# Optimization experiments

Measured on AMD Instinct MI355X. Metric: run time of the kernel, lower is better.

## Reference

```python
import jax, jax.numpy as jnp
import numpy as np

B, L, H, W = 16, 4096, 64, 64
SEQ = 1024  # target_sequence_length (hardcoded in the torch module)
SP = 32     # sqrt(SEQ)


def _conv1d(x, w, b, pad):
    y = jax.lax.conv_general_dilated(x, w, (1,), [(pad, pad)],
                                     dimension_numbers=('NCH', 'OIH', 'NCH'))
    return y + b[None, :, None]


def _conv2d(x, w, b, pad, groups=1):
    y = jax.lax.conv_general_dilated(x, w, (1, 1), [(pad, pad)] * 2,
                                     feature_group_count=groups,
                                     dimension_numbers=('NCHW', 'OIHW', 'NCHW'))
    return y + b[None, :, None, None]


def _forward(us_input, img_input, us_w1, us_b1, us_w2, us_b2, us_w3, us_b3,
             aff_w, aff_w_high, aff_thr, img_w1, img_b1, img_w2, img_b2, img_w3, img_b3,
             db_qkv_w, db_qkv_b, db_dw_w, db_dw_b, db_proj_w, db_proj_b,
             db_fc_w, db_fc_b, db_dep_w, db_dep_b, db_temp,
             ca_qkv_w, ca_qkv_b, ca_out_w, ca_out_b,
             tf_ch1_w, tf_ch1_b, tf_ch2_w, tf_ch2_b,
             tf_sp1_w, tf_sp1_b, tf_sp2_w, tf_sp2_b, cls_w, cls_b):
    b = us_input.shape[0]
    # ---- ultrasound 1D conv branch ----
    x = us_input.transpose(0, 2, 1)                    # [B,1,L]
    x = jax.nn.relu(_conv1d(x, us_w1, us_b1, 1))
    x = jax.nn.relu(_conv1d(x, us_w2, us_b2, 1))
    x = jax.nn.relu(_conv1d(x, us_w3, us_b3, 1))
    us_feat = x.transpose(0, 2, 1)                     # [B,L,64]
    # ---- adaptive frequency filtering (training-mode high-freq mask included) ----
    n = us_feat.shape[1]
    xf = jnp.fft.rfft(us_feat, axis=1, norm='ortho')   # [B,Nf,64] complex
    w_c = aff_w[:, 0] + 1j * aff_w[:, 1]
    xw = xf * w_c
    energy = jnp.sum(jnp.abs(xf) ** 2, axis=-1)        # [B,Nf]
    med = jnp.median(energy.reshape(b, -1), axis=1, keepdims=True)
    ne = energy / (med + 1e-6)
    hard = (ne > aff_thr).astype(jnp.float32)
    mask = jax.lax.stop_gradient(hard - aff_thr) + aff_thr  # straight-through threshold
    wh_c = aff_w_high[:, 0] + 1j * aff_w_high[:, 1]
    xw = xw + (xf * mask[..., None]) * wh_c
    us_feat = jnp.fft.irfft(xw, n=n, axis=1, norm='ortho')  # [B,L,64]
    # ---- image 2D conv branch ----
    y = jax.nn.relu(_conv2d(img_input, img_w1, img_b1, 1))
    y = jax.nn.relu(_conv2d(y, img_w2, img_b2, 1))
    y = jax.nn.relu(_conv2d(y, img_w3, img_b3, 1))     # [B,64,H,W]
    # ---- dual-branch feature fusion block ----
    hgt, wid = y.shape[2], y.shape[3]
    hw = hgt * wid
    qkv = jnp.einsum('oi,bihw->bohw', db_qkv_w, y) + db_qkv_b[None, :, None, None]
    qkv = _conv2d(qkv, db_dw_w, db_dw_b, 1, groups=192)      # depthwise (3x3x3 conv @ D=1 -> center 3x3)
    # convolutional branch: faithful row-major reshape as in torch
    f_all = qkv.reshape(b, hw, 12, 16).transpose(0, 2, 1, 3)  # [B,12,HW,16]
    f_all = jnp.einsum('oi,bink->bonk', db_fc_w, f_all) + db_fc_b[None, :, None, None]
    f_conv = f_all.transpose(0, 3, 1, 2).reshape(b, 144, hgt, wid)
    out_conv = _conv2d(f_conv, db_dep_w, db_dep_b, 1, groups=16)  # [B,64,H,W]
    # channel attention branch
    q, k, v = jnp.split(qkv, 3, axis=1)
    q = q.reshape(b, 4, 16, hw)
    k = k.reshape(b, 4, 16, hw)
    v = v.reshape(b, 4, 16, hw)
    q = q / jnp.maximum(jnp.linalg.norm(q, axis=-1, keepdims=True), 1e-12)
    k = k / jnp.maximum(jnp.linalg.norm(k, axis=-1, keepdims=True), 1e-12)
    attn = jax.nn.softmax(jnp.einsum('bhcn,bhdn->bhcd', q, k) * db_temp, axis=-1)
    out = jnp.einsum('bhcd,bhdn->bhcn', attn, v).reshape(b, 64, hgt, wid)
    out = jnp.einsum('oi,bihw->bohw', db_proj_w, out) + db_proj_b[None, :, None, None]
    img_feat = (out + out_conv).reshape(b, 64, hw).transpose(0, 2, 1)  # [B,HW,64]
    # ---- adaptive avg pool to SEQ (lengths divide evenly) ----
    us_red = us_feat.transpose(0, 2, 1).reshape(b, 64, SEQ, -1).mean(-1).transpose(0, 2, 1)
    img_red = img_feat.transpose(0, 2, 1).reshape(b, 64, SEQ, -1).mean(-1).transpose(0, 2, 1)
    # ---- cross-modal attention (shared qkv/out projections) ----
    def heads(t):
        u = (jnp.einsum('bli,oi->blo', t, ca_qkv_w) + ca_qkv_b).reshape(b, SEQ, 4, 3, 16)
        return (u[:, :, :, 0].transpose(0, 2, 1, 3),
                u[:, :, :, 1].transpose(0, 2, 1, 3),
                u[:, :, :, 2].transpose(0, 2, 1, 3))
    q1, k1, v1 = heads(us_red)
    q2, k2, v2 = heads(img_red)
    scale = 1.0 / jnp.sqrt(jnp.float32(16.0))
    a1 = jax.nn.softmax(jnp.einsum('bhqd,bhkd->bhqk', q1, k2) * scale, axis=-1)
    a2 = jax.nn.softmax(jnp.einsum('bhqd,bhkd->bhqk', q2, k1) * scale, axis=-1)
    o1 = jnp.einsum('bhqk,bhkd->bhqd', a1, v2).transpose(0, 2, 1, 3).reshape(b, SEQ, 64)
    o2 = jnp.einsum('bhqk,bhkd->bhqd', a2, v1).transpose(0, 2, 1, 3).reshape(b, SEQ, 64)
    o1 = jnp.einsum('bli,oi->blo', o1, ca_out_w) + ca_out_b
    o2 = jnp.einsum('bli,oi->blo', o2, ca_out_w) + ca_out_b
    t1 = o1.transpose(0, 2, 1).reshape(b, 64, SP, SP)
    t2 = o2.transpose(0, 2, 1).reshape(b, 64, SP, SP)
    # ---- modal fusion attention (channel + spatial gating) ----
    ch_pool = jnp.stack([t1.mean((2, 3)), t1.max((2, 3)), t2.mean((2, 3)), t2.max((2, 3))], axis=1)  # [B,4,64]
    c1 = _conv1d(ch_pool, tf_ch1_w, tf_ch1_b, 1)      # [B,1,64]
    c2 = _conv1d(ch_pool, tf_ch2_w, tf_ch2_b, 1)
    ch_stack = jax.nn.softmax(jnp.stack([c1, c2], 0), axis=0)      # [2,B,1,64]
    ch_stack = ch_stack.transpose(0, 1, 3, 2)[..., None]           # [2,B,64,1,1]
    sp_pool = jnp.concatenate([t1.mean(1, keepdims=True), t1.max(1, keepdims=True),
                               t2.mean(1, keepdims=True), t2.max(1, keepdims=True)], axis=1)
    s1 = _conv2d(sp_pool, tf_sp1_w, tf_sp1_b, 3)
    s2 = _conv2d(sp_pool, tf_sp2_w, tf_sp2_b, 3)
    sp_stack = jax.nn.softmax(jnp.stack([s1, s2], 0), axis=0)      # [2,B,1,SP,SP]
    att = ch_stack + sp_stack + 1.0                                # [2,B,64,SP,SP]
    fuse = att[0] * t1 + att[1] * t2
    logits = fuse.mean((2, 3)) @ cls_w.T + cls_b
    return jax.nn.softmax(logits, axis=1)


def setup_inputs() -> dict:
    key = jax.random.key(0)
    ks = iter(jax.random.split(key, 64))
    def rn(shape, s=0.2):
        return jax.random.normal(next(ks), shape, dtype=jnp.float32) * s
    d = {
        'us_input': jax.random.normal(next(ks), (B, L, 1), dtype=jnp.float32),
        'img_input': jax.random.normal(next(ks), (B, 3, H, W), dtype=jnp.float32),
        'us_w1': rn((16, 1, 3)), 'us_b1': rn((16,), 0.02),
        'us_w2': rn((32, 16, 3)), 'us_b2': rn((32,), 0.02),
        'us_w3': rn((64, 32, 3)), 'us_b3': rn((64,), 0.02),
        'aff_w': rn((64, 2), 0.02), 'aff_w_high': rn((64, 2), 0.02),
        'aff_thr': jax.random.uniform(next(ks), (1,), dtype=jnp.float32),
        'img_w1': rn((16, 3, 3, 3)), 'img_b1': rn((16,), 0.02),
        'img_w2': rn((32, 16, 3, 3)), 'img_b2': rn((32,), 0.02),
        'img_w3': rn((64, 32, 3, 3)), 'img_b3': rn((64,), 0.02),
        'db_qkv_w': rn((192, 64), 0.1), 'db_qkv_b': rn((192,), 0.02),
        'db_dw_w': rn((192, 1, 3, 3)), 'db_dw_b': rn((192,), 0.02),
        'db_proj_w': rn((64, 64), 0.1), 'db_proj_b': rn((64,), 0.02),
        'db_fc_w': rn((9, 12), 0.1), 'db_fc_b': rn((9,), 0.02),
        'db_dep_w': rn((64, 9, 3, 3), 0.1), 'db_dep_b': rn((64,), 0.02),
        'db_temp': jnp.ones((4, 1, 1), dtype=jnp.float32),
        'ca_qkv_w': rn((192, 64), 0.1), 'ca_qkv_b': rn((192,), 0.02),
        'ca_out_w': rn((64, 64), 0.1), 'ca_out_b': rn((64,), 0.02),
        'tf_ch1_w': rn((1, 4, 3)), 'tf_ch1_b': rn((1,), 0.02),
        'tf_ch2_w': rn((1, 4, 3)), 'tf_ch2_b': rn((1,), 0.02),
        'tf_sp1_w': rn((1, 4, 7, 7)), 'tf_sp1_b': rn((1,), 0.02),
        'tf_sp2_w': rn((1, 4, 7, 7)), 'tf_sp2_b': rn((1,), 0.02),
        'cls_w': rn((9, 64), 0.1), 'cls_b': rn((9,), 0.02),
    }
    return d


def reference(us_input, img_input, us_w1, us_b1, us_w2, us_b2, us_w3, us_b3,
              aff_w, aff_w_high, aff_thr, img_w1, img_b1, img_w2, img_b2, img_w3, img_b3,
              db_qkv_w, db_qkv_b, db_dw_w, db_dw_b, db_proj_w, db_proj_b,
              db_fc_w, db_fc_b, db_dep_w, db_dep_b, db_temp,
              ca_qkv_w, ca_qkv_b, ca_out_w, ca_out_b,
              tf_ch1_w, tf_ch1_b, tf_ch2_w, tf_ch2_b,
              tf_sp1_w, tf_sp1_b, tf_sp2_w, tf_sp2_b, cls_w, cls_b):
    return _forward(us_input, img_input, us_w1, us_b1, us_w2, us_b2, us_w3, us_b3,
                    aff_w, aff_w_high, aff_thr, img_w1, img_b1, img_w2, img_b2, img_w3, img_b3,
                    db_qkv_w, db_qkv_b, db_dw_w, db_dw_b, db_proj_w, db_proj_b,
                    db_fc_w, db_fc_b, db_dep_w, db_dep_b, db_temp,
                    ca_qkv_w, ca_qkv_b, ca_out_w, ca_out_b,
                    tf_ch1_w, tf_ch1_b, tf_ch2_w, tf_ch2_b,
                    tf_sp1_w, tf_sp1_b, tf_sp2_w, tf_sp2_b, cls_w, cls_b)
```

## Files before the change

### kernel.cpp

```cpp
#include <hip/hip_runtime.h>

typedef float v2f __attribute__((ext_vector_type(2)));

static constexpr size_t O_SMALL   = 0;
static constexpr size_t O_US3     = 3145728;
static constexpr size_t O_XF      = 7340032;
static constexpr size_t O_USFILT  = 11536384;
static constexpr size_t O_ENERGY  = 15730688;
static constexpr size_t O_MED     = 15764480;
static constexpr size_t O_NRM     = 15765504;
static constexpr size_t O_ATTNS   = 15767552;
static constexpr size_t O_CHPOOL  = 15783936;
static constexpr size_t O_CHW     = 15788032;
static constexpr size_t O_SPPOOL  = 15790080;
static constexpr size_t O_SPW     = 15855616;
static constexpr size_t O_QKV     = 15888384;
static constexpr size_t O_QKVDW   = 28471296;
static constexpr size_t O_OUTCONV = 41054208;
static constexpr size_t CA_USRED = 0, CA_IMGRED = 1, CA_Q1 = 2, CA_K1 = 3, CA_V1 = 4,
                        CA_Q2 = 5, CA_K2 = 6, CA_V2 = 7, CA_O1 = 8, CA_O2 = 9,
                        CA_T1 = 10, CA_T2 = 11;


template<int Ci, int Co>
// ... 73 lines not shown
#pragma unroll
    for (int j = 0; j < N; ++j) acc[j] = bias;
    const float* wb = w + co * Ci * 9;
    for (int ci = 0; ci < Ci; ++ci) {
        float wr[9];
#pragma unroll
        for (int k = 0; k < 9; ++k) wr[k] = wb[ci * 9 + k];
#pragma unroll
        for (int dy = 0; dy < 3; ++dy) {
            const float* lr = &lds[ci][ysub + dy][x0];
            float a = lr[0], bb = lr[1];
#pragma unroll
            for (int j = 0; j < N; ++j) {
                float cc = lr[2 + j];
                acc[j] += wr[dy * 3] * a + wr[dy * 3 + 1] * bb + wr[dy * 3 + 2] * cc;
                a = bb; bb = cc;
            }
        }
    }
    float* ob = out + ((size_t)b * Co + co) * 4096 + (y0 + ysub) * 64 + x0;
#pragma unroll
    for (int j = 0; j < N; ++j) ob[j] = fmaxf(acc[j], 0.f);
}

__device__ __forceinline__ void fft4096_r4_sb(float2* A, int tid)
{
    int Ns = 1;
    for (int s = 0; s < 6; ++s) {
        float cfac = -0.25f / (float)Ns;
        float2 va[4][4];
#pragma unroll
        for (int r = 0; r < 4; ++r) {
            int j = (r << 8) + tid;
            va[r][0] = A[j];
            va[r][1] = A[j + 1024];
            va[r][2] = A[j + 2048];
            va[r][3] = A[j + 3072];
        }
        __syncthreads();
#pragma unroll
        for (int r = 0; r < 4; ++r) {
            int j = (r << 8) + tid;
            int jm = j & (Ns - 1);
            float rev = (float)jm * cfac;
            float s1 = __builtin_amdgcn_sinf(rev);
            float c1 = __builtin_amdgcn_cosf(rev);
            float c2 = c1 * c1 - s1 * s1, s2 = 2.f * c1 * s1;
            float c3 = c2 * c1 - s2 * s1, s3 = c2 * s1 + s2 * c1;
            float2 v0 = va[r][0], v1 = va[r][1], v2 = va[r][2], v3 = va[r][3];
            float2 u1 = make_float2(v1.x * c1 - v1.y * s1, v1.x * s1 + v1.y * c1);
            float2 u2 = make_float2(v2.x * c2 - v2.y * s2, v2.x * s2 + v2.y * c2);
            float2 u3 = make_float2(v3.x * c3 - v3.y * s3, v3.x * s3 + v3.y * c3);
            float t0x = v0.x + u2.x, t0y = v0.y + u2.y;
            float t1x = v0.x - u2.x, t1y = v0.y - u2.y;
            float t2x = u1.x + u3.x, t2y = u1.y + u3.y;
            float t3x = u1.x - u3.x, t3y = u1.y - u3.y;
            int base = ((j - jm) << 2) + jm;
            A[base]          = make_float2(t0x + t2x, t0y + t2y);
            A[base + Ns]     = make_float2(t1x + t3y, t1y - t3x);
            A[base + 2 * Ns] = make_float2(t0x - t2x, t0y - t2y);
            A[base + 3 * Ns] = make_float2(t1x - t3y, t1y + t3x);
        }
        __syncthreads();
        Ns <<= 2;
    }
}

__device__ __forceinline__ void fft_fwd_body(char* smem_raw, int row,
    const float* __restrict__ us3, float* __restrict__ xf)
{
    float2* A = (float2*)smem_raw;
    int tid = threadIdx.x;
    const float* x = us3 + (size_t)row * 4096;
    for (int r = 0; r < 16; ++r) {
        int i = (r << 8) + tid;
        A[i] = make_float2(x[i], 0.f);
    }
    __syncthreads();
    fft4096_r4_sb(A, tid);
    float* out = xf + (size_t)row * 4098;
    for (int r = 0; r < 9; ++r) {
        int f = (r << 8) + tid;
        if (f < 2049) {
            out[2 * f]     = A[f].x * (1.f / 64.f);
            out[2 * f + 1] = A[f].y * (1.f / 64.f);
        }
    }
}

__device__ __forceinline__ void energy_body(int bid,
    const float* __restrict__ xf, float* __restrict__ energy)
{
    int idx = bid * 256 + threadIdx.x;
    if (idx >= 16 * 2049) return;
    int b = idx / 2049, f = idx % 2049;
    const float* p = xf + (size_t)b * 64 * 4098 + 2 * f;
    float e = 0.f;
    for (int ch = 0; ch < 64; ++ch) {
        float re = p[0], im = p[1];
        e += re * re + im * im;
        p += 4098;
    }
    energy[idx] = e;
}

__device__ __forceinline__ void median_body(char* smem_raw, int b,
    const float* __restrict__ energy, float* __restrict__ med)
{
    float* s = (float*)smem_raw;
    int tid = threadIdx.x;
    for (int r = 0; r < 16; ++r) {
        int i = (r << 8) + tid;
        s[i] = (i < 2049) ? energy[b * 2049 + i] : 3.0e38f;
    }
    __syncthreads();
    for (int k = 2; k <= 4096; k <<= 1) {
        for (int j = k >> 1; j > 0; j >>= 1) {
            for (int r = 0; r < 16; ++r) {
                int i = (r << 8) + tid;
                int ixj = i ^ j;
                if (ixj > i) {
                    bool up = ((i & k) == 0);
                    float a = s[i], bb = s[ixj];
                    if ((a > bb) == up) { s[i] = bb; s[ixj] = a; }
                }
            }
            __syncthreads();
        }
    }
    if (tid == 0) med[b] = s[1024];
}

__device__ __forceinline__ void filter_ifft_body(char* smem_raw, int row,
    const float* __restrict__ xf, const float* __restrict__ energy,
    const float* __restrict__ med, const float* __restrict__ aff_w,
    const float* __restrict__ aff_wh, const float* __restrict__ thr_p,
    float* __restrict__ us_filt)
{
    float2* A = (float2*)smem_raw;
    int b = row >> 6, ch = row & 63;
    int tid = threadIdx.x;
    float thr = thr_p[0];
    float mden = med[b] + 1e-6f;
    float w0r = aff_w[2 * ch], w0i = aff_w[2 * ch + 1];
    float whr = aff_wh[2 * ch], whi = aff_wh[2 * ch + 1];
    const float* X = xf + (size_t)row * 4098;
    const float* E = energy + b * 2049;
    for (int r = 0; r < 9; ++r) {
        int f = (r << 8) + tid;
        if (f < 2049) {
            float re = X[2 * f], im = X[2 * f + 1];
            float mask = (E[f] / mden > thr) ? 1.f : 0.f;
            float wr = w0r + mask * whr;
            float wi = w0i + mask * whi;
            float xr = re * wr - im * wi;
            float xi = re * wi + im * wr;
            A[f] = make_float2(xr, -xi);
            if (f >= 1 && f <= 2047) A[4096 - f] = make_float2(xr, xi);
        }
    }
    __syncthreads();
    fft4096_r4_sb(A, tid);
    float* out = us_filt + (size_t)row * 4096;
    for (int r = 0; r < 16; ++r) {
        int i = (r << 8) + tid;
        out[i] = A[i].x * (1.f / 64.f);
    }
}

__device__ __forceinline__ void qkv1x1_body(int bid, const float* __restrict__ y,
    const float* __restrict__ w, const float* __restrict__ bs, float* __restrict__ out)
{
    int oc = bid & 3;
    int pc = (bid >> 2) & 15;
    int b  = bid >> 6;
    int p = pc * 256 + threadIdx.x;
    const float* inb = y + (size_t)b * 262144 + p;
    v2f reg[32];
#pragma unroll
    for (int ci = 0; ci < 32; ++ci) {
        v2f r; r.x = inb[(2 * ci) * 4096]; r.y = inb[(2 * ci + 1) * 4096];
        reg[ci] = r;
    }
    float* ob = out + (size_t)b * 786432 + (size_t)oc * 48 * 4096 + p;
    for (int o = 0; o < 48; ++o) {
        const v2f* wr = (const v2f*)(w + (oc * 48 + o) * 64);
        v2f s2 = {0.f, 0.f};
#pragma unroll
        for (int ci = 0; ci < 32; ++ci) s2 = wr[ci] * reg[ci] + s2;
        ob[o * 4096] = bs[oc * 48 + o] + s2.x + s2.y;
    }
}

__device__ __forceinline__ void dwconv_body(int bid, const float* __restrict__ in,
    const float* __restrict__ w, const float* __restrict__ bs, float* __restrict__ out)
{
    int idx = bid * 256 + threadIdx.x;
    int x = idx & 63, yy = (idx >> 6) & 63;
    int c = (idx >> 12) % 192;
    const float* p = in + idx;
    const float* wp = w + c * 9;
    float acc = bs[c];
    bool ym = yy > 0, yp = yy < 63, xm = x > 0, xp = x < 63;
    float s = wp[4] * p[0];
    if (ym) { s += wp[1] * p[-64]; if (xm) s += wp[0] * p[-65]; if (xp) s += wp[2] * p[-63]; }
    if (xm) s += wp[3] * p[-1];
    if (xp) s += wp[5] * p[1];
    if (yp) { s += wp[7] * p[64];  if (xm) s += wp[6] * p[63];  if (xp) s += wp[8] * p[65]; }
    out[idx] = acc + s;
}

__device__ __forceinline__ void fc_body(int bid, const float* __restrict__ qkv_dw,
    const float* __restrict__ fw, const float* __restrict__ fb, float* __restrict__ fcv)
{
    int idx = bid * 256 + threadIdx.x;
    int k = idx & 15;
    int p = (idx >> 4) & 4095;
    int b = idx >> 16;
    const float* base = qkv_dw + (size_t)b * 786432;
    float u[12];
#pragma unroll
    for (int i = 0; i < 12; ++i) u[i] = base[p * 192 + i * 16 + k];
#pragma unroll
    for (int o = 0; o < 9; ++o) {
        float s = fb[o];
#pragma unroll
        for (int i = 0; i < 12; ++i) s += fw[o * 12 + i] * u[i];
        fcv[(((size_t)b * 16 + k) * 9 + o) * 4096 + p] = s;
    }
}

__device__ __forceinline__ void depconv2_body(char* smem_raw, int bid,
    const float* __restrict__ fcv, const float* __restrict__ w,
    const float* __restrict__ bs, float* __restrict__ out)
{
    auto lds = (float(*)[10][66])smem_raw;
    int band = bid & 7;
    int g    = (bid >> 3) & 15;
    int b    = bid >> 7;
    int y0 = band * 8;
    int tid = threadIdx.x;
    const float* inb = fcv + ((size_t)(b * 16 + g) * 9) * 4096;
    for (int i = tid; i < 9 * 10 * 64; i += 256) {
        int x  = i & 63;
        int ry = (i >> 6) % 10;
        int ci = i / 640;
        int gy = y0 - 1 + ry;
        lds[ci][ry][x + 1] = (gy >= 0 && gy < 64) ? inb[ci * 4096 + gy * 64 + x] : 0.f;
    }
    for (int i = tid; i < 90; i += 256) {
        int ry = i % 10, ci = i / 10;
        lds[ci][ry][0] = 0.f; lds[ci][ry][65] = 0.f;
    }
    __syncthreads();
    int co   = tid >> 6;
    int ysub = (tid >> 3) & 7;
    int x0   = (tid & 7) * 8;
    int ocg  = g * 4 + co;
    float acc[8];
    float bias = bs[ocg];
#pragma unroll
    for (int j = 0; j < 8; ++j) acc[j] = bias;
    const float* wb = w + ocg * 81;
    for (int ci = 0; ci < 9; ++ci) {
        float wr[9];
#pragma unroll
        for (int k = 0; k < 9; ++k) wr[k] = wb[ci * 9 + k];
#pragma unroll
        for (int dy = 0; dy < 3; ++dy) {
            const float* lr = &lds[ci][ysub + dy][x0];
            float a = lr[0], bb = lr[1];
#pragma unroll
            for (int j = 0; j < 8; ++j) {
                float cc = lr[2 + j];
                acc[j] += wr[dy * 3] * a + wr[dy * 3 + 1] * bb + wr[dy * 3 + 2] * cc;
                a = bb; bb = cc;
            }
        }
    }
    float* ob = out + ((size_t)b * 64 + ocg) * 4096 + (y0 + ysub) * 64 + x0;
#pragma unroll
    for (int j = 0; j < 8; ++j) ob[j] = acc[j];
}

__device__ __forceinline__ void qknorm_body(char* smem_raw, int row,
    const float* __restrict__ qkv_dw, float* __restrict__ nrm)
{
    float* red = (float*)smem_raw;
    int which = row >> 10;
    int r = row & 1023;
    int b = r >> 6, hd = r & 63;
    const float* p = qkv_dw + ((size_t)b * 192 + which * 64 + hd) * 4096;
    float s = 0.f;
    for (int i = threadIdx.x; i < 4096; i += 256) { float v = p[i]; s += v * v; }
    red[threadIdx.x] = s;
    __syncthreads();
    for (int st = 128; st > 0; st >>= 1) {
        if (threadIdx.x < st) red[threadIdx.x] += red[threadIdx.x + st];
        __syncthreads();
    }
    if (threadIdx.x == 0) nrm[row] = sqrtf(red[0]);
}

__device__ __forceinline__ void chpool2_body(int bid, const float* __restrict__ t1,
    const float* __restrict__ t2, float* __restrict__ chpool)
{
    int rg = bid & 15;
    int b  = bid >> 4;
    int wave = threadIdx.x >> 6, lane = threadIdx.x & 63;
    int c = rg * 4 + wave;
    const float* p1 = t1 + ((size_t)b * 64 + c) * 1024;
    const float* p2 = t2 + ((size_t)b * 64 + c) * 1024;
    float m1 = 0.f, x1 = -3e38f, m2 = 0.f, x2 = -3e38f;
#pragma unroll
    for (int i = 0; i < 16; ++i) {
        int p = lane + i * 64;
        float a = p1[p], bb = p2[p];
        m1 += a; x1 = fmaxf(x1, a);
        m2 += bb; x2 = fmaxf(x2, bb);
    }
    for (int off = 32; off > 0; off >>= 1) {
        m1 += __shfl_xor(m1, off);
        x1 = fmaxf(x1, __shfl_xor(x1, off));
        m2 += __shfl_xor(m2, off);
        x2 = fmaxf(x2, __shfl_xor(x2, off));
    }
    if (lane == 0) {
        chpool[b * 256 + c]       = m1 * (1.f / 1024.f);
        chpool[b * 256 + 64 + c]  = x1;
        chpool[b * 256 + 128 + c] = m2 * (1.f / 1024.f);
        chpool[b * 256 + 192 + c] = x2;
    }
}

__device__ __forceinline__ void sppool_body(int bid, const float* __restrict__ t1,
    const float* __restrict__ t2, float* __restrict__ sppool)
{
    int b = bid >> 2;
    int p = (bid & 3) * 256 + threadIdx.x;
    float m1 = 0.f, x1 = -3e38f, m2 = 0.f, x2 = -3e38f;
    const float* p1 = t1 + (size_t)b * 65536 + p;
    const float* p2 = t2 + (size_t)b * 65536 + p;
    for (int c = 0; c < 64; ++c) {
        float a = p1[c * 1024], bb = p2[c * 1024];
        m1 += a; x1 = fmaxf(x1, a);
        m2 += bb; x2 = fmaxf(x2, bb);
    }
    sppool[b * 4096 + p]        = m1 * (1.f / 64.f);
    sppool[b * 4096 + 1024 + p] = x1;
    sppool[b * 4096 + 2048 + p] = m2 * (1.f / 64.f);
    sppool[b * 4096 + 3072 + p] = x2;
}

__device__ __forceinline__ void chgate_body(int b, const float* __restrict__ chpool,
    const float* __restrict__ w1, const float* __restrict__ b1,
    const float* __restrict__ w2, const float* __restrict__ b2, float* __restrict__ chw)
{
    int c = threadIdx.x;
    if (c >= 64) return;
    float a1 = b1[0], a2 = b2[0];
    for (int ic = 0; ic < 4; ++ic) {
        const float* cp = chpool + b * 256 + ic * 64;
        for (int d = -1; d <= 1; ++d) {
            int cc = c + d;
            if (cc >= 0 && cc < 64) {
                a1 += w1[ic * 3 + d + 1] * cp[cc];
                a2 += w2[ic * 3 + d + 1] * cp[cc];
            }
        }
    }
    float mx = fmaxf(a1, a2);
    float e1 = __expf(a1 - mx), e2 = __expf(a2 - mx);
    float inv = 1.f / (e1 + e2);
    chw[b * 64 + c]        = e1 * inv;
    chw[1024 + b * 64 + c] = e2 * inv;
}

__device__ __forceinline__ void spgate_body(int bid, const float* __restrict__ sppool,
    const float* __restrict__ w1, const float* __restrict__ b1,
    const float* __restrict__ w2, const float* __restrict__ b2, float* __restrict__ spw)
{
    int idx = bid * 256 + threadIdx.x;
    int p = idx & 1023;
    int b = idx >> 10;
    int y = p >> 5, x = p & 31;
    float a1 = b1[0], a2 = b2[0];
    for (int ic = 0; ic < 4; ++ic) {
        const float* sp = sppool + b * 4096 + ic * 1024;
        for (int dy = -3; dy <= 3; ++dy) {
            int yy = y + dy;
            if (yy < 0 || yy > 31) continue;
            for (int dx = -3; dx <= 3; ++dx) {
                int xx = x + dx;
                if (xx < 0 || xx > 31) continue;
                float v = sp[yy * 32 + xx];
                int wi = ic * 49 + (dy + 3) * 7 + (dx + 3);
                a1 += w1[wi] * v;
                a2 += w2[wi] * v;
            }
        }
    }
    float mx = fmaxf(a1, a2);
    float e1 = __expf(a1 - mx), e2 = __expf(a2 - mx);
    float inv = 1.f / (e1 + e2);
    spw[idx]         = e1 * inv;
    spw[16384 + idx] = e2 * inv;
}


__global__ __launch_bounds__(256) void s1_kernel(const float* us_in, const float* uw, const float* ub,
    float* uo, const float* iin, const float* iw, const float* ib, float* io)
{
    __shared__ __align__(16) char smem[3168];
    if (blockIdx.x < 512) conv1d3_body<1, 16>(smem, blockIdx.x, us_in, uw, ub, uo);
    else                  conv2d3_body<3, 16, 2>(smem, blockIdx.x - 512, iin, iw, ib, io);
}

__global__ __launch_bounds__(256) void s2_kernel(const float* ui, const float* uw, const float* ub,
    float* uo, const float* ii, const float* iw, const float* ib, float* io)
{
    __shared__ __align__(16) char smem[16896];
    if (blockIdx.x < 512) conv1d3_body<16, 32>(smem, blockIdx.x, ui, uw, ub, uo);
    else                  conv2d3_body<16, 32, 2>(smem, blockIdx.x - 512, ii, iw, ib, io);
}

__global__ __launch_bounds__(256) void s3_kernel(const float* ui, const float* uw, const float* ub,
    float* uo, const float* ii, const float* iw, const float* ib, float* io)
{
    __shared__ __align__(16) char smem[33792];
    if (blockIdx.x < 512) conv1d3_body<32, 64>(smem, blockIdx.x, ui, uw, ub, uo);
    else                  conv2d3_body<32, 64, 2>(smem, blockIdx.x - 512, ii, iw, ib, io);
}

__global__ __launch_bounds__(256) void s4_kernel(const float* us3, float* xf,
    const float* y, const float* qw, const float* qb, float* qkv)
{
    __shared__ __align__(16) char smem[32768];
    if (blockIdx.x < 1024) fft_fwd_body(smem, blockIdx.x, us3, xf);
    else                   qkv1x1_body(blockIdx.x - 1024, y, qw, qb, qkv);
}

__global__ __launch_bounds__(256) void s5_kernel(const float* qkv, const float* dww,
    const float* dwb, float* qkv_dw, const float* xf, float* energy)
{
    if (blockIdx.x < 49152) dwconv_body(blockIdx.x, qkv, dww, dwb, qkv_dw);
    else                    energy_body(blockIdx.x - 49152, xf, energy);
}

__global__ __launch_bounds__(256) void s6_kernel(const float* qkv_dw, const float* fw,
    const float* fb, float* fcv, const float* energy, float* med)
{
    __shared__ __align__(16) char smem[16384];
    if (blockIdx.x < 4096) fc_body(blockIdx.x, qkv_dw, fw, fb, fcv);
    else                   median_body(smem, blockIdx.x - 4096, energy, med);
}

__global__ __launch_bounds__(256) void s7a_kernel(const float* fcv, const float* dw,
    const float* db, float* out_conv, const float* qkv_dw, float* nrm)
{
    __shared__ __align__(16) char smem[23808];
    if (blockIdx.x < 2048) depconv2_body(smem, blockIdx.x, fcv, dw, db, out_conv);
    else                   qknorm_body(smem, blockIdx.x - 2048, qkv_dw, nrm);
}

__global__ __launch_bounds__(256) void filt_kernel(const float* xf, const float* energy,
    const float* med, const float* aw, const float* awh, const float* thr, float* us_filt)
{
    __shared__ __align__(16) char smem[32768];
    filter_ifft_body(smem, blockIdx.x, xf, energy, med, aw, awh, thr, us_filt);
}

__global__ __launch_bounds__(256) void s16_kernel(const float* t1, const float* t2,
    float* chpool, float* sppool)
{
    if (blockIdx.x < 256) chpool2_body(blockIdx.x, t1, t2, chpool);
    else                  sppool_body(blockIdx.x - 256, t1, t2, sppool);
}

__global__ __launch_bounds__(256) void s17_kernel(const float* sppool, const float* sw1,
    const float* sb1, const float* sw2, const float* sb2, float* spw,
    const float* chpool, const float* cw1, const float* cb1, const float* cw2,
    const float* cb2, float* chw)
{
    if (blockIdx.x < 64) spgate_body(blockIdx.x, sppool, sw1, sb1, sw2, sb2, spw);
    else                 chgate_body(blockIdx.x - 64, chpool, cw1, cb1, cw2, cb2, chw);
}


__global__ __launch_bounds__(256) void chan_attn_part_kernel(
    const float* __restrict__ qkv_dw, float* __restrict__ part)
{
    int blk = blockIdx.x;
    int nc = blk & 7;
    int bh = blk >> 3;
    int b = bh >> 2, h = bh & 3;
    __shared__ float Qs[16][130];
    __shared__ float Ks2[16][130];
    int c = threadIdx.x >> 4, d = threadIdx.x & 15;
    const float* qbase = qkv_dw + ((size_t)b * 192 + h * 16) * 4096 + nc * 512;
    const float* kbase = qkv_dw + ((size_t)b * 192 + 64 + h * 16) * 4096 + nc * 512;
    float s = 0.f;
    for (int n0 = 0; n0 < 512; n0 += 128) {
        __syncthreads();
        for (int r = 0; r < 8; ++r) {
            int i = (r << 8) + threadIdx.x;
            int row = i >> 7, col = i & 127;
            Qs[row][col]  = qbase[(size_t)row * 4096 + n0 + col];
            Ks2[row][col] = kbase[(size_t)row * 4096 + n0 + col];
        }
        __syncthreads();
#pragma unroll 8
        for (int n = 0; n < 128; ++n) s += Qs[c][n] * Ks2[d][n];
    }
    part[(size_t)blk * 256 + threadIdx.x] = s;
}

__global__ __launch_bounds__(256) void chan_attn_merge_kernel(
    const float* __restrict__ part, const float* __restrict__ nrm,
    const float* __restrict__ temp, float* __restrict__ attn_s)
{
    int bh = blockIdx.x;
    int b = bh >> 2, h = bh & 3;
    int c = threadIdx.x >> 4, d = threadIdx.x & 15;
    float s = 0.f;
#pragma unroll
    for (int i = 0; i < 8; ++i) s += part[(size_t)(bh * 8 + i) * 256 + threadIdx.x];
    float nq = fmaxf(nrm[b * 64 + h * 16 + c], 1e-12f);
    float nk = fmaxf(nrm[1024 + b * 64 + h * 16 + d], 1e-12f);
    s = s / (nq * nk) * temp[h];
    __shared__ float S[16][17];
    S[c][d] = s;
    __syncthreads();
    if (threadIdx.x < 16) {
        int cc = threadIdx.x;
        float mx = -3e30f;
        for (int dd = 0; dd < 16; ++dd) mx = fmaxf(mx, S[cc][dd]);
        float sm = 0.f;
        float e[16];
        for (int dd = 0; dd < 16; ++dd) { e[dd] = __expf(S[cc][dd] - mx); sm += e[dd]; }
        float inv = 1.f / sm;
        float* dst = attn_s + (size_t)bh * 256 + cc * 16;
        for (int dd = 0; dd < 16; ++dd) dst[dd] = e[dd] * inv;
    }
}


__global__ __launch_bounds__(256, 2) void attnproj_kernel(const float* __restrict__ attn_s,
    const float* __restrict__ qkv_dw, const float* __restrict__ outconv,
    const float* __restrict__ pw, const float* __restrict__ pb, float* __restrict__ img_feat)
{
    int blk = blockIdx.x;
    int oc = blk & 1;
    int pc = (blk >> 1) & 15;
    int b  = blk >> 5;
    int n = pc * 256 + threadIdx.x;
    const float* vb = qkv_dw + ((size_t)b * 192 + 128) * 4096 + n;
    v2f v[32];
#pragma unroll
    for (int i = 0; i < 32; ++i) {
        v2f r; r.x = vb[(2 * i) * 4096]; r.y = vb[(2 * i + 1) * 4096];
        v[i] = r;
    }
    const float* ab = attn_s + (size_t)b * 1024;
    for (int h = 0; h < 4; ++h) {
        v2f tmp[8];
#pragma unroll
        for (int c2 = 0; c2 < 8; ++c2) {
            v2f s2a = {0.f, 0.f}, s2b = {0.f, 0.f};
            const v2f* r0 = (const v2f*)(ab + (h * 16 + 2 * c2) * 16);
            const v2f* r1 = (const v2f*)(ab + (h * 16 + 2 * c2 + 1) * 16);
#pragma unroll
            for (int d2 = 0; d2 < 8; ++d2) {
                s2a = r0[d2] * v[h * 8 + d2] + s2a;
                s2b = r1[d2] * v[h * 8 + d2] + s2b;
            }
            v2f t; t.x = s2a.x + s2a.y; t.y = s2b.x + s2b.y;
            tmp[c2] = t;
        }
#pragma unroll
        for (int c2 = 0; c2 < 8; ++c2) v[h * 8 + c2] = tmp[c2];
    }
    float* ofb = img_feat + (size_t)b * 262144 + (size_t)oc * 32 * 4096 + n;
    const float* ocb = outconv + (size_t)b * 262144 + (size_t)oc * 32 * 4096 + n;
    for (int o = 0; o < 32; ++o) {
        const v2f* wr = (const v2f*)(pw + (oc * 32 + o) * 64);
        v2f s2 = {0.f, 0.f};
#pragma unroll
        for (int c2 = 0; c2 < 32; ++c2) s2 = wr[c2] * v[c2] + s2;
        ofb[o * 4096] = pb[oc * 32 + o] + ocb[o * 4096] + s2.x + s2.y;
    }
}

__global__ __launch_bounds__(256) void poolred_kernel(const float* __restrict__ us_filt,
    const float* __restrict__ img_feat, float* __restrict__ us_redT, float* __restrict__ img_redT)
{
    int idx = blockIdx.x * 256 + threadIdx.x;
    int s4 = idx & 1023;
    int c = (idx >> 10) & 63;
    int b = (idx >> 16) & 15;
    int m = idx >> 20;
    const float* in = (m ? img_feat : us_filt) + ((size_t)b * 64 + c) * 4096 + s4 * 4;
    float4 v4 = *(const float4*)in;
    float v = 0.25f * (v4.x + v4.y + v4.z + v4.w);
    (m ? img_redT : us_redT)[((size_t)b * 64 + c) * 1024 + s4] = v;
}

__global__ __launch_bounds__(256, 2) void caqkv2_kernel(const float* __restrict__ us_redT,
    const float* __restrict__ img_redT, const float* __restrict__ qw, const float* __restrict__ qb,
    float* __restrict__ q1, float* __restrict__ k1, float* __restrict__ v1,
    float* __restrict__ q2, float* __restrict__ k2, float* __restrict__ v2)
{
    int blk = blockIdx.x;
    int h  = blk & 3;
    int pc = (blk >> 2) & 3;
    int b  = (blk >> 4) & 15;
    int m  = blk >> 8;
    int l = pc * 256 + threadIdx.x;
    const float* in = (m ? img_redT : us_redT) + (size_t)b * 65536 + l;
    v2f reg[32];
#pragma unroll
    for (int i = 0; i < 32; ++i) {
        v2f r; r.x = in[(2 * i) * 1024]; r.y = in[(2 * i + 1) * 1024];
        reg[i] = r;
    }
    size_t rowoff = ((size_t)(b * 4 + h) * 1024 + l) * 16;
    float* dst[3] = { (m ? q2 : q1) + rowoff, (m ? k2 : k1) + rowoff, (m ? v2 : v1) + rowoff };
#pragma unroll
    for (int which = 0; which < 3; ++which) {
        float* dp = dst[which];
        for (int d = 0; d < 16; ++d) {
            int o = h * 48 + which * 16 + d;
            const v2f* wr = (const v2f*)(qw + o * 64);
            v2f s2 = {0.f, 0.f};
#pragma unroll
            for (int i = 0; i < 32; ++i) s2 = wr[i] * reg[i] + s2;
            dp[d] = qb[o] + s2.x + s2.y;
        }
    }
}

__global__ __launch_bounds__(256) void kmax_kernel(const float* __restrict__ k1,
    const float* __restrict__ k2, float* __restrict__ kmax)
{
    int unit = blockIdx.x;
    int h = unit & 3, m = (unit >> 2) & 1, b = unit >> 3;
    const float* K = m ? k1 : k2;
    const float* Kb = K + (size_t)(b * 4 + h) * 16384;
    int tid = threadIdx.x;
    float mx = 0.f;
#pragma unroll
    for (int j = 0; j < 4; ++j) {
        const float* kp = Kb + (size_t)(tid + 256 * j) * 16;
        float s = 0.f;
#pragma unroll
        for (int d = 0; d < 16; ++d) s += kp[d] * kp[d];
        mx = fmaxf(mx, s);
    }
    for (int off = 32; off > 0; off >>= 1) mx = fmaxf(mx, __shfl_xor(mx, off));
    __shared__ float red[4];
    if ((tid & 63) == 0) red[tid >> 6] = mx;
    __syncthreads();
    if (tid == 0) {
        float r = fmaxf(fmaxf(red[0], red[1]), fmaxf(red[2], red[3]));
        kmax[unit] = sqrtf(r);
    }
}

__global__ __launch_bounds__(256, 2) void cross_attn8_kernel(
    const float* __restrict__ q1, const float* __restrict__ k1, const float* __restrict__ v1,
    const float* __restrict__ q2, const float* __restrict__ k2, const float* __restrict__ v2,
    const float* __restrict__ kmax, float* __restrict__ ls_, float* __restrict__ accp)
{
    int blk  = blockIdx.x;
    int kt   = blk & 7;
    int unit = blk >> 3;
    int h = unit & 3;
    int m = (unit >> 2) & 1;
    int b = unit >> 3;
    const float* Q = m ? q2 : q1;
    const float* K = m ? k1 : k2;
    const float* V = m ? v1 : v2;
    const float* Qb = Q + (size_t)(b * 4 + h) * 16384;
    const float* Kb = K + (size_t)(b * 4 + h) * 16384 + kt * 128 * 16;
    const float* Vb = V + (size_t)(b * 4 + h) * 16384 + kt * 128 * 16;
    int tid = threadIdx.x;
    const float SC = 0.25f * 1.44269504088896340736f;
    float km = kmax[unit];
    v2f qr[4][8], acc[4][8];
    float M[4], ls[4];
#pragma unroll
    for (int j = 0; j < 4; ++j) {
        const v2f* qp = (const v2f*)(Qb + (size_t)(tid + 256 * j) * 16);
        v2f qs2 = {0.f, 0.f};
#pragma unroll
        for (int i = 0; i < 8; ++i) {
            v2f q = qp[i];
            qs2 = q * q + qs2;
            qr[j][i] = q * SC;
        }
        M[j] = sqrtf(qs2.x + qs2.y) * km * SC;
        ls[j] = 0.f;
#pragma unroll
        for (int i = 0; i < 8; ++i) acc[j][i] = (v2f){0.f, 0.f};
    }
    __shared__ float Ks[64 * 16];
    __shared__ float Vs[64 * 16];
    for (int t0 = 0; t0 < 128; t0 += 64) {
        __syncthreads();
        ((float4*)Ks)[tid] = ((const float4*)(Kb + t0 * 16))[tid];
        ((float4*)Vs)[tid] = ((const float4*)(Vb + t0 * 16))[tid];
        __syncthreads();
#pragma unroll 2
        for (int t = 0; t < 64; ++t) {
            const v2f* k2p = (const v2f*)&Ks[t * 16];
            v2f kk[8];
#pragma unroll
            for (int i = 0; i < 8; ++i) kk[i] = k2p[i];
            float p[4];
#pragma unroll
            for (int j = 0; j < 4; ++j) {
                v2f s2 = {0.f, 0.f};
#pragma unroll
                for (int i = 0; i < 8; ++i) s2 = qr[j][i] * kk[i] + s2;
                p[j] = exp2f(s2.x + s2.y - M[j]);
                ls[j] += p[j];
            }
            const v2f* v2p = (const v2f*)&Vs[t * 16];
            v2f vv[8];
#pragma unroll
            for (int i = 0; i < 8; ++i) vv[i] = v2p[i];
#pragma unroll
            for (int j = 0; j < 4; ++j) {
                v2f pj = {p[j], p[j]};
#pragma unroll
                for (int i = 0; i < 8; ++i) acc[j][i] = pj * vv[i] + acc[j][i];
            }
        }
    }
#pragma unroll
    for (int j = 0; j < 4; ++j) {
        int q = tid + 256 * j;
        size_t pi = (size_t)(unit * 8 + kt) * 1024 + q;
        ls_[pi] = ls[j];
        v2f* ap = (v2f*)(accp + pi * 16);
#pragma unroll
        for (int i = 0; i < 8; ++i) ap[i] = acc[j][i];
    }
}

__global__ __launch_bounds__(256) void ca_merge3_kernel(const float* __restrict__ ls_,
    const float* __restrict__ accp, float* __restrict__ o1t, float* __restrict__ o2t)
{
    int idx = blockIdx.x * 256 + threadIdx.x;
    int q = idx & 1023;
    int unit = idx >> 10;
    int h = unit & 3;
    int m = (unit >> 2) & 1;
    int b = unit >> 3;
    float l = 0.f;
#pragma unroll
    for (int i = 0; i < 8; ++i) l += ls_[(size_t)(unit * 8 + i) * 1024 + q];
    float inv = 1.f / l;
    float* dst = (m ? o2t : o1t) + (size_t)b * 65536 + (size_t)(h * 16) * 1024 + q;
#pragma unroll
    for (int d = 0; d < 16; ++d) {
        float s = 0.f;
#pragma unroll
        for (int i = 0; i < 8; ++i) s += accp[((size_t)(unit * 8 + i) * 1024 + q) * 16 + d];
        dst[d * 1024] = s * inv;
    }
}

__global__ __launch_bounds__(256, 2) void caout2_kernel(const float* __restrict__ o1t,
    const float* __restrict__ o2t, const float* __restrict__ ow, const float* __restrict__ ob_,
    float* __restrict__ t1, float* __restrict__ t2)
{
    int blk = blockIdx.x;
    int oc = blk & 1;
    int pc = (blk >> 1) & 3;
    int b  = (blk >> 3) & 15;
    int m  = blk >> 7;
    int l = pc * 256 + threadIdx.x;
    const float* in = (m ? o2t : o1t) + (size_t)b * 65536 + l;
    v2f reg[32];
#pragma unroll
    for (int i = 0; i < 32; ++i) {
        v2f r; r.x = in[(2 * i) * 1024]; r.y = in[(2 * i + 1) * 1024];
        reg[i] = r;
    }
    float* t = (m ? t2 : t1) + (size_t)b * 65536 + (size_t)oc * 32 * 1024 + l;
    for (int o = 0; o < 32; ++o) {
        const v2f* wr = (const v2f*)(ow + (oc * 32 + o) * 64);
        v2f s2 = {0.f, 0.f};
#pragma unroll
        for (int i = 0; i < 32; ++i) s2 = wr[i] * reg[i] + s2;
        t[o * 1024] = ob_[oc * 32 + o] + s2.x + s2.y;
    }
}

__global__ __launch_bounds__(256) void final2_kernel(const float* __restrict__ t1,
    const float* __restrict__ t2, const float* __restrict__ chw, const float* __restrict__ spw,
    const float* __restrict__ clsw, const float* __restrict__ clsb, float* __restrict__ out)
{
    int b = blockIdx.x;
    int wave = threadIdx.x >> 6, lane = threadIdx.x & 63;
    __shared__ float feat[64];
    __shared__ float lg[9];
    const float* s1 = spw + b * 1024;
    const float* s2 = spw + 16384 + b * 1024;
    for (int round = 0; round < 16; ++round) {
        int c = round * 4 + wave;
        float g1 = chw[b * 64 + c] + 1.f;
        float g2 = chw[1024 + b * 64 + c] + 1.f;
        const float* p1 = t1 + ((size_t)b * 64 + c) * 1024;
        const float* p2 = t2 + ((size_t)b * 64 + c) * 1024;
        float acc = 0.f;
#pragma unroll
        for (int i = 0; i < 16; ++i) {
            int p = lane + i * 64;
            acc += (g1 + s1[p]) * p1[p] + (g2 + s2[p]) * p2[p];
        }
        for (int off = 32; off > 0; off >>= 1) acc += __shfl_xor(acc, off);
        if (lane == 0) feat[c] = acc * (1.f / 1024.f);
    }
    __syncthreads();
    if (threadIdx.x < 9) {
        int c = threadIdx.x;
        float s = clsb[c];
        for (int i = 0; i < 64; ++i) s += clsw[c * 64 + i] * feat[i];
        lg[c] = s;
    }
    __syncthreads();
    if (threadIdx.x == 0) {
        float mx = -3e38f;
        for (int o = 0; o < 9; ++o) mx = fmaxf(mx, lg[o]);
        float sm = 0.f;
        float e[9];
        for (int o = 0; o < 9; ++o) { e[o] = __expf(lg[o] - mx); sm += e[o]; }
        float inv = 1.f / sm;
        for (int o = 0; o < 9; ++o) out[b * 9 + o] = e[o] * inv;
    }
}

extern "C" void kernel_launch(void* const* d_in, const int* in_sizes, int n_in,
                              void* d_out, int out_size, void* d_ws, size_t ws_size,
                              hipStream_t stream)
{
    (void)in_sizes; (void)n_in; (void)out_size; (void)ws_size;
    const float* us_input = (const float*)d_in[0];
    const float* img_input = (const float*)d_in[1];
    const float* us_w1 = (const float*)d_in[2];  const float* us_b1 = (const float*)d_in[3];
    const float* us_w2 = (const float*)d_in[4];  const float* us_b2 = (const float*)d_in[5];
    const float* us_w3 = (const float*)d_in[6];  const float* us_b3 = (const float*)d_in[7];
    const float* aff_w = (const float*)d_in[8];  const float* aff_wh = (const float*)d_in[9];
    const float* aff_thr = (const float*)d_in[10];
    const float* img_w1 = (const float*)d_in[11]; const float* img_b1 = (const float*)d_in[12];
    const float* img_w2 = (const float*)d_in[13]; const float* img_b2 = (const float*)d_in[14];
    const float* img_w3 = (const float*)d_in[15]; const float* img_b3 = (const float*)d_in[16];
    const float* db_qkv_w = (const float*)d_in[17]; const float* db_qkv_b = (const float*)d_in[18];
    const float* db_dw_w = (const float*)d_in[19];  const float* db_dw_b = (const float*)d_in[20];
    const float* db_proj_w = (const float*)d_in[21]; const float* db_proj_b = (const float*)d_in[22];
    const float* db_fc_w = (const float*)d_in[23];  const float* db_fc_b = (const float*)d_in[24];
    const float* db_dep_w = (const float*)d_in[25]; const float* db_dep_b = (const float*)d_in[26];
    const float* db_temp = (const float*)d_in[27];
    const float* ca_qkv_w = (const float*)d_in[28]; const float* ca_qkv_b = (const float*)d_in[29];
    const float* ca_out_w = (const float*)d_in[30]; const float* ca_out_b = (const float*)d_in[31];
    const float* tf_ch1_w = (const float*)d_in[32]; const float* tf_ch1_b = (const float*)d_in[33];
    const float* tf_ch2_w = (const float*)d_in[34]; const float* tf_ch2_b = (const float*)d_in[35];
    const float* tf_sp1_w = (const float*)d_in[36]; const float* tf_sp1_b = (const float*)d_in[37];
    const float* tf_sp2_w = (const float*)d_in[38]; const float* tf_sp2_b = (const float*)d_in[39];
    const float* cls_w = (const float*)d_in[40];   const float* cls_b = (const float*)d_in[41];

    float* ws = (float*)d_ws;
    float* us1     = ws + O_SMALL;
    float* us2     = ws + O_SMALL + 1048576;
    float* us3     = ws + O_US3;
    float* xf      = ws + O_XF;
    float* us_filt = ws + O_USFILT;
    float* energy  = ws + O_ENERGY;
    float* med     = ws + O_MED;
    float* nrm     = ws + O_NRM;
    float* attn_s  = ws + O_ATTNS;
    float* chpool  = ws + O_CHPOOL;
    float* chw     = ws + O_CHW;
    float* sppool  = ws + O_SPPOOL;
    float* spw     = ws + O_SPW;
    float* qkv     = ws + O_QKV;
    float* qkv_dw  = ws + O_QKVDW;
    float* out_conv= ws + O_OUTCONV;
    float* img1 = ws + O_USFILT;
    float* img2 = ws + O_USFILT + 1048576;
    float* y = ws + O_QKVDW;
    float* fcv = qkv;
    float* img_feat = xf;
    float* ca_part = ws + O_XF + 3000000;
    float* us_redT  = ws + O_QKV + CA_USRED  * 1048576;
    float* img_redT = ws + O_QKV + CA_IMGRED * 1048576;
    float* q1 = ws + O_QKV + CA_Q1 * 1048576;
    float* k1 = ws + O_QKV + CA_K1 * 1048576;
    float* v1 = ws + O_QKV + CA_V1 * 1048576;
    float* q2 = ws + O_QKV + CA_Q2 * 1048576;
    float* k2 = ws + O_QKV + CA_K2 * 1048576;
    float* v2 = ws + O_QKV + CA_V2 * 1048576;
    float* o1t = ws + O_QKV + CA_O1 * 1048576;
    float* o2t = ws + O_QKV + CA_O2 * 1048576;
    float* t1 = ws + O_QKV + CA_T1 * 1048576;
    float* t2 = ws + O_QKV + CA_T2 * 1048576;
    float* ca_accp = ws + O_QKVDW;
    float* ca_ls   = ws + O_US3;
    float* ca_kmax = ws + O_US3 + 1048576;

    s1_kernel<<<1024, 256, 0, stream>>>(us_input, us_w1, us_b1, us1,
                                        img_input, img_w1, img_b1, img1);
    s2_kernel<<<1024, 256, 0, stream>>>(us1, us_w2, us_b2, us2,
                                        img1, img_w2, img_b2, img2);
    s3_kernel<<<1024, 256, 0, stream>>>(us2, us_w3, us_b3, us3,
                                        img2, img_w3, img_b3, y);
    s4_kernel<<<2048, 256, 0, stream>>>(us3, xf, y, db_qkv_w, db_qkv_b, qkv);
    s5_kernel<<<49281, 256, 0, stream>>>(qkv, db_dw_w, db_dw_b, qkv_dw, xf, energy);
    s6_kernel<<<4112, 256, 0, stream>>>(qkv_dw, db_fc_w, db_fc_b, fcv, energy, med);
    s7a_kernel<<<4096, 256, 0, stream>>>(fcv, db_dep_w, db_dep_b, out_conv, qkv_dw, nrm);
    filt_kernel<<<1024, 256, 0, stream>>>(xf, energy, med, aff_w, aff_wh, aff_thr, us_filt);
    chan_attn_part_kernel<<<512, 256, 0, stream>>>(qkv_dw, ca_part);
    chan_attn_merge_kernel<<<64, 256, 0, stream>>>(ca_part, nrm, db_temp, attn_s);
    attnproj_kernel<<<512, 256, 0, stream>>>(attn_s, qkv_dw, out_conv, db_proj_w, db_proj_b, img_feat);
    poolred_kernel<<<8192, 256, 0, stream>>>(us_filt, img_feat, us_redT, img_redT);
    caqkv2_kernel<<<512, 256, 0, stream>>>(us_redT, img_redT, ca_qkv_w, ca_qkv_b,
                                           q1, k1, v1, q2, k2, v2);
    kmax_kernel<<<128, 256, 0, stream>>>(k1, k2, ca_kmax);
    cross_attn8_kernel<<<1024, 256, 0, stream>>>(q1, k1, v1, q2, k2, v2, ca_kmax, ca_ls, ca_accp);
    ca_merge3_kernel<<<512, 256, 0, stream>>>(ca_ls, ca_accp, o1t, o2t);
    caout2_kernel<<<256, 256, 0, stream>>>(o1t, o2t, ca_out_w, ca_out_b, t1, t2);
    s16_kernel<<<320, 256, 0, stream>>>(t1, t2, chpool, sppool);
    s17_kernel<<<80, 256, 0, stream>>>(sppool, tf_sp1_w, tf_sp1_b, tf_sp2_w, tf_sp2_b, spw,
                                       chpool, tf_ch1_w, tf_ch1_b, tf_ch2_w, tf_ch2_b, chw);
    final2_kernel<<<16, 256, 0, stream>>>(t1, t2, chw, spw, cls_w, cls_b, (float*)d_out);
}
```

Baseline: 912.2 us.

## Merge stage kernels and replace split-K cross-attention merge with atomics

Folds the channel-attention partial kernel into s6, and the filter/iFFT kernel into s7 alongside depconv and qk-norm, cutting launch count and letting independent work share a grid. The cross-attention kernel now accumulates its unnormalized outputs and softmax denominators directly into global buffers with atomicAdd, instead of writing per-split partials that a separate merge kernel reduced. Normalization moves into the output-projection kernel, and a new zero kernel clears the accumulators first. This removes the large partial-buffer round trip, but adds atomic contention across the 8 key splits and makes the float summation order nondeterministic.

Result: faster. 865.5 us (-5.1%).

```diff
diff --git a/kernel.cpp b/kernel.cpp
--- a/kernel.cpp
+++ b/kernel.cpp
@@ -399,6 +399,33 @@
     if (threadIdx.x == 0) nrm[row] = sqrtf(red[0]);
 }
 
+__device__ __forceinline__ void chan_attn_part_body(char* smem_raw, int blk,
+    const float* __restrict__ qkv_dw, float* __restrict__ part)
+{
+    auto Qs  = (float(*)[130])smem_raw;
+    auto Ks2 = (float(*)[130])(smem_raw + 16 * 130 * 4);
+    int nc = blk & 7;
+    int bh = blk >> 3;
+    int b = bh >> 2, h = bh & 3;
+    int c = threadIdx.x >> 4, d = threadIdx.x & 15;
+    const float* qbase = qkv_dw + ((size_t)b * 192 + h * 16) * 4096 + nc * 512;
+    const float* kbase = qkv_dw + ((size_t)b * 192 + 64 + h * 16) * 4096 + nc * 512;
+    float s = 0.f;
+    for (int n0 = 0; n0 < 512; n0 += 128) {
+        __syncthreads();
+        for (int r = 0; r < 8; ++r) {
+            int i = (r << 8) + threadIdx.x;
+            int row = i >> 7, col = i & 127;
+            Qs[row][col]  = qbase[(size_t)row * 4096 + n0 + col];
+            Ks2[row][col] = kbase[(size_t)row * 4096 + n0 + col];
+        }
+        __syncthreads();
+#pragma unroll 8
+        for (int n = 0; n < 128; ++n) s += Qs[c][n] * Ks2[d][n];
+    }
+    part[(size_t)blk * 256 + threadIdx.x] = s;
+}
+
 __device__ __forceinline__ void chpool2_body(int bid, const float* __restrict__ t1,
     const float* __restrict__ t2, float* __restrict__ chpool)
 {
@@ -545,26 +572,30 @@
 }
 
 __global__ __launch_bounds__(256) void s6_kernel(const float* qkv_dw, const float* fw,
-    const float* fb, float* fcv, const float* energy, float* med)
-{
-    __shared__ __align__(16) char smem[16384];
-    if (blockIdx.x < 4096) fc_body(blockIdx.x, qkv_dw, fw, fb, fcv);
-    else                   median_body(smem, blockIdx.x - 4096, energy, med);
-}
-
-__global__ __launch_bounds__(256) void s7a_kernel(const float* fcv, const float* dw,
-    const float* db, float* out_conv, const float* qkv_dw, float* nrm)
-{
-    __shared__ __align__(16) char smem[23808];
-    if (blockIdx.x < 2048) depconv2_body(smem, blockIdx.x, fcv, dw, db, out_conv);
-    else                   qknorm_body(smem, blockIdx.x - 2048, qkv_dw, nrm);
-}
-
-__global__ __launch_bounds__(256) void filt_kernel(const float* xf, const float* energy,
-    const float* med, const float* aw, const float* awh, const float* thr, float* us_filt)
+    const float* fb, float* fcv, const float* energy, float* med, float* part)
+{
+    __shared__ __align__(16) char smem[16640];
+    if (blockIdx.x < 4096)      fc_body(blockIdx.x, qkv_dw, fw, fb, fcv);
+    else if (blockIdx.x < 4112) median_body(smem, blockIdx.x - 4096, energy, med);
+    else                        chan_attn_part_body(smem, blockIdx.x - 4112, qkv_dw, part);
+}
+
+__global__ __launch_bounds__(256) void s7_kernel(const float* fcv, const float* dw,
+    const float* db, float* out_conv, const float* qkv_dw, float* nrm,
+    const float* xf, const float* energy, const float* med, const float* aw,
+    const float* awh, const float* thr, float* us_filt)
 {
     __shared__ __align__(16) char smem[32768];
-    filter_ifft_body(smem, blockIdx.x, xf, energy, med, aw, awh, thr, us_filt);
+    if (blockIdx.x < 2048)      depconv2_body(smem, blockIdx.x, fcv, dw, db, out_conv);
+    else if (blockIdx.x < 4096) qknorm_body(smem, blockIdx.x - 2048, qkv_dw, nrm);
+    else                        filter_ifft_body(smem, blockIdx.x - 4096, xf, energy, med, aw, awh, thr, us_filt);
+}
+
+__global__ __launch_bounds__(256) void zero_kernel(float* o1t, float* o2t, float* lsg)
+{
+    int idx = blockIdx.x * 256 + threadIdx.x;
+    if (idx < 1048576) { o1t[idx] = 0.f; o2t[idx] = 0.f; }
+    if (idx < 131072) lsg[idx] = 0.f;
 }
 
 __global__ __launch_bounds__(256) void s16_kernel(const float* t1, const float* t2,
@@ -581,35 +612,6 @@
 {
     if (blockIdx.x < 64) spgate_body(blockIdx.x, sppool, sw1, sb1, sw2, sb2, spw);
     else                 chgate_body(blockIdx.x - 64, chpool, cw1, cb1, cw2, cb2, chw);
-}
-
-
-__global__ __launch_bounds__(256) void chan_attn_part_kernel(
-    const float* __restrict__ qkv_dw, float* __restrict__ part)
-{
-    int blk = blockIdx.x;
-    int nc = blk & 7;
-    int bh = blk >> 3;
-    int b = bh >> 2, h = bh & 3;
-    __shared__ float Qs[16][130];
-    __shared__ float Ks2[16][130];
-    int c = threadIdx.x >> 4, d = threadIdx.x & 15;
-    const float* qbase = qkv_dw + ((size_t)b * 192 + h * 16) * 4096 + nc * 512;
-    const float* kbase = qkv_dw + ((size_t)b * 192 + 64 + h * 16) * 4096 + nc * 512;
-    float s = 0.f;
-    for (int n0 = 0; n0 < 512; n0 += 128) {
-        __syncthreads();
-        for (int r = 0; r < 8; ++r) {
-            int i = (r << 8) + threadIdx.x;
-            int row = i >> 7, col = i & 127;
-            Qs[row][col]  = qbase[(size_t)row * 4096 + n0 + col];
-            Ks2[row][col] = kbase[(size_t)row * 4096 + n0 + col];
-        }
-        __syncthreads();
-#pragma unroll 8
-        for (int n = 0; n < 128; ++n) s += Qs[c][n] * Ks2[d][n];
-    }
-    part[(size_t)blk * 256 + threadIdx.x] = s;
 }
 
 __global__ __launch_bounds__(256) void chan_attn_merge_kernel(
@@ -763,10 +765,11 @@
     }
 }
 
-__global__ __launch_bounds__(256, 2) void cross_attn8_kernel(
+__global__ __launch_bounds__(256, 2) void cross_attn9_kernel(
     const float* __restrict__ q1, const float* __restrict__ k1, const float* __restrict__ v1,
     const float* __restrict__ q2, const float* __restrict__ k2, const float* __restrict__ v2,
-    const float* __restrict__ kmax, float* __restrict__ ls_, float* __restrict__ accp)
+    const float* __restrict__ kmax, float* __restrict__ ls_glob,
+    float* __restrict__ o1t, float* __restrict__ o2t)
 {
     int blk  = blockIdx.x;
     int kt   = blk & 7;
@@ -834,42 +837,23 @@
             }
         }
     }
+    float* obase = (m ? o2t : o1t) + (size_t)b * 65536 + (size_t)(h * 16) * 1024;
 #pragma unroll
     for (int j = 0; j < 4; ++j) {
         int q = tid + 256 * j;
-        size_t pi = (size_t)(unit * 8 + kt) * 1024 + q;
-        ls_[pi] = ls[j];
-        v2f* ap = (v2f*)(accp + pi * 16);
-#pragma unroll
-        for (int i = 0; i < 8; ++i) ap[i] = acc[j][i];
-    }
-}
-
-__global__ __launch_bounds__(256) void ca_merge3_kernel(const float* __restrict__ ls_,
-    const float* __restrict__ accp, float* __restrict__ o1t, float* __restrict__ o2t)
-{
-    int idx = blockIdx.x * 256 + threadIdx.x;
-    int q = idx & 1023;
-    int unit = idx >> 10;
-    int h = unit & 3;
-    int m = (unit >> 2) & 1;
-    int b = unit >> 3;
-    float l = 0.f;
-#pragma unroll
-    for (int i = 0; i < 8; ++i) l += ls_[(size_t)(unit * 8 + i) * 1024 + q];
-    float inv = 1.f / l;
-    float* dst = (m ? o2t : o1t) + (size_t)b * 65536 + (size_t)(h * 16) * 1024 + q;
-#pragma unroll
-    for (int d = 0; d < 16; ++d) {
-        float s = 0.f;
-#pragma unroll
-        for (int i = 0; i < 8; ++i) s += accp[((size_t)(unit * 8 + i) * 1024 + q) * 16 + d];
-        dst[d * 1024] = s * inv;
-    }
-}
-
-__global__ __launch_bounds__(256, 2) void caout2_kernel(const float* __restrict__ o1t,
-    const float* __restrict__ o2t, const float* __restrict__ ow, const float* __restrict__ ob_,
+        atomicAdd(&ls_glob[(size_t)unit * 1024 + q], ls[j]);
+        float* onum = obase + q;
+#pragma unroll
+        for (int i = 0; i < 8; ++i) {
+            atomicAdd(&onum[(2 * i) * 1024], acc[j][i].x);
+            atomicAdd(&onum[(2 * i + 1) * 1024], acc[j][i].y);
+        }
+    }
+}
+
+__global__ __launch_bounds__(256, 2) void caout3_kernel(const float* __restrict__ o1t,
+    const float* __restrict__ o2t, const float* __restrict__ ls_glob,
+    const float* __restrict__ ow, const float* __restrict__ ob_,
     float* __restrict__ t1, float* __restrict__ t2)
 {
     int blk = blockIdx.x;
@@ -878,11 +862,16 @@
     int b  = (blk >> 3) & 15;
     int m  = blk >> 7;
     int l = pc * 256 + threadIdx.x;
+    float inv[4];
+#pragma unroll
+    for (int h = 0; h < 4; ++h)
+        inv[h] = 1.f / ls_glob[(size_t)(b * 8 + m * 4 + h) * 1024 + l];
     const float* in = (m ? o2t : o1t) + (size_t)b * 65536 + l;
     v2f reg[32];
 #pragma unroll
     for (int i = 0; i < 32; ++i) {
-        v2f r; r.x = in[(2 * i) * 1024]; r.y = in[(2 * i + 1) * 1024];
+        float iv = inv[i >> 3];
+        v2f r; r.x = in[(2 * i) * 1024] * iv; r.y = in[(2 * i + 1) * 1024] * iv;
         reg[i] = r;
     }
     float* t = (m ? t2 : t1) + (size_t)b * 65536 + (size_t)oc * 32 * 1024 + l;
@@ -990,7 +979,7 @@
     float* y = ws + O_QKVDW;
     float* fcv = qkv;
     float* img_feat = xf;
-    float* ca_part = ws + O_XF + 3000000;
+    float* ca_part = ws + O_SMALL;
     float* us_redT  = ws + O_QKV + CA_USRED  * 1048576;
     float* img_redT = ws + O_QKV + CA_IMGRED * 1048576;
     float* q1 = ws + O_QKV + CA_Q1 * 1048576;
@@ -1003,7 +992,6 @@
     float* o2t = ws + O_QKV + CA_O2 * 1048576;
     float* t1 = ws + O_QKV + CA_T1 * 1048576;
     float* t2 = ws + O_QKV + CA_T2 * 1048576;
-    float* ca_accp = ws + O_QKVDW;
     float* ca_ls   = ws + O_US3;
     float* ca_kmax = ws + O_US3 + 1048576;
 
@@ -1015,19 +1003,20 @@
                                         img2, img_w3, img_b3, y);
     s4_kernel<<<2048, 256, 0, stream>>>(us3, xf, y, db_qkv_w, db_qkv_b, qkv);
     s5_kernel<<<49281, 256, 0, stream>>>(qkv, db_dw_w, db_dw_b, qkv_dw, xf, energy);
-    s6_kernel<<<4112, 256, 0, stream>>>(qkv_dw, db_fc_w, db_fc_b, fcv, energy, med);
-    s7a_kernel<<<4096, 256, 0, stream>>>(fcv, db_dep_w, db_dep_b, out_conv, qkv_dw, nrm);
-    filt_kernel<<<1024, 256, 0, stream>>>(xf, energy, med, aff_w, aff_wh, aff_thr, us_filt);
-    chan_attn_part_kernel<<<512, 256, 0, stream>>>(qkv_dw, ca_part);
+    s6_kernel<<<4624, 256, 0, stream>>>(qkv_dw, db_fc_w, db_fc_b, fcv, energy, med, ca_part);
+    s7_kernel<<<5120, 256, 0, stream>>>(fcv, db_dep_w, db_dep_b, out_conv,
+                                        qkv_dw, nrm, xf, energy, med,
+                                        aff_w, aff_wh, aff_thr, us_filt);
+    zero_kernel<<<4096, 256, 0, stream>>>(o1t, o2t, ca_ls);
     chan_attn_merge_kernel<<<64, 256, 0, stream>>>(ca_part, nrm, db_temp, attn_s);
     attnproj_kernel<<<512, 256, 0, stream>>>(attn_s, qkv_dw, out_conv, db_proj_w, db_proj_b, img_feat);
     poolred_kernel<<<8192, 256, 0, stream>>>(us_filt, img_feat, us_redT, img_redT);
     caqkv2_kernel<<<512, 256, 0, stream>>>(us_redT, img_redT, ca_qkv_w, ca_qkv_b,
                                            q1, k1, v1, q2, k2, v2);
     kmax_kernel<<<128, 256, 0, stream>>>(k1, k2, ca_kmax);
-    cross_attn8_kernel<<<1024, 256, 0, stream>>>(q1, k1, v1, q2, k2, v2, ca_kmax, ca_ls, ca_accp);
-    ca_merge3_kernel<<<512, 256, 0, stream>>>(ca_ls, ca_accp, o1t, o2t);
-    caout2_kernel<<<256, 256, 0, stream>>>(o1t, o2t, ca_out_w, ca_out_b, t1, t2);
+    cross_attn9_kernel<<<1024, 256, 0, stream>>>(q1, k1, v1, q2, k2, v2, ca_kmax,
+                                                 ca_ls, o1t, o2t);
+    caout3_kernel<<<256, 256, 0, stream>>>(o1t, o2t, ca_ls, ca_out_w, ca_out_b, t1, t2);
     s16_kernel<<<320, 256, 0, stream>>>(t1, t2, chpool, sppool);
     s17_kernel<<<80, 256, 0, stream>>>(sppool, tf_sp1_w, tf_sp1_b, tf_sp2_w, tf_sp2_b, spw,
                                        chpool, tf_ch1_w, tf_ch1_b, tf_ch2_w, tf_ch2_b, chw);
```
